# Optimization experiments

Hardware: AMD Instinct MI355X
Metric: run time of the kernel (lower is better)

Reference implementation:

```python
import jax, jax.numpy as jnp
import numpy as np

B, T, D = 2, 2048, 2048
H, KVH, HD = 32, 8, 64
N_REP = H // KVH


def setup_inputs() -> dict:
    key = jax.random.key(0)
    ks = jax.random.split(key, 7)
    x = jax.random.normal(ks[0], (B, T, D), dtype=jnp.float32)
    # rope tables: [max_seq, head_dim//2]
    cos = jax.random.uniform(ks[1], (T, HD // 2), dtype=jnp.float32, minval=-1.0, maxval=1.0)
    sin = jax.random.uniform(ks[2], (T, HD // 2), dtype=jnp.float32, minval=-1.0, maxval=1.0)
    s = 0.02
    wq = jax.random.normal(ks[3], (D, H * HD), dtype=jnp.float32) * s
    wk = jax.random.normal(ks[4], (D, KVH * HD), dtype=jnp.float32) * s
    wv = jax.random.normal(ks[5], (D, KVH * HD), dtype=jnp.float32) * s
    wo = jax.random.normal(ks[6], (H * HD, D), dtype=jnp.float32) * s
    return {"x": x, "cos": cos, "sin": sin, "wq": wq, "wk": wk, "wv": wv, "wo": wo}


def _rotate(t):
    h = t.shape[-1] // 2
    return jnp.concatenate([-t[..., h:], t[..., :h]], axis=-1)


def reference(x, cos, sin, wq, wk, wv, wo):
    b, t, _ = x.shape
    # projections -> [B, heads, T, HD]
    q = (x @ wq).reshape(b, t, H, HD).transpose(0, 2, 1, 3)
    k = (x @ wk).reshape(b, t, KVH, HD).transpose(0, 2, 1, 3)
    v = (x @ wv).reshape(b, t, KVH, HD).transpose(0, 2, 1, 3)
    # rope: cos/sin tiled (concat) to full head_dim, broadcast over batch/head
    cos_f = jnp.tile(cos[:t], (1, 2))[None, None]  # [1,1,T,HD]
    sin_f = jnp.tile(sin[:t], (1, 2))[None, None]
    q = q * cos_f + _rotate(q) * sin_f
    k = k * cos_f + _rotate(k) * sin_f
    # GQA: repeat kv heads
    k = jnp.repeat(k, N_REP, axis=1)
    v = jnp.repeat(v, N_REP, axis=1)
    scale = 1.0 / np.sqrt(HD).astype(np.float32)
    scores = jnp.einsum('bhqd,bhkd->bhqk', q, k) * scale
    causal = jnp.tril(jnp.ones((t, t), dtype=bool))
    scores = jnp.where(causal, scores, jnp.float32(-1e30))
    attn = jax.nn.softmax(scores, axis=-1)
    out = jnp.einsum('bhqk,bhkd->bhqd', attn, v)
    out = out.transpose(0, 2, 1, 3).reshape(b, t, H * HD)
    return out @ wo
```

## Files before the change

kernel.cpp:

```cpp
#include <hip/hip_runtime.h>
#include <hip/hip_bf16.h>
#include <cstdint>

typedef unsigned short u16;
typedef unsigned int u32;
typedef __bf16 bf16x8 __attribute__((ext_vector_type(8)));
typedef float f32x4 __attribute__((ext_vector_type(4)));
typedef float f32x16 __attribute__((ext_vector_type(16)));

#define BATCH 2
#define SEQ 2048
#define DMODEL 2048
#define NH 32
#define NKVH 8
#define HD 64
#define NQROWS (BATCH*SEQ)
#define QCOLS (NH*HD)
#define KVCOLS (NKVH*HD)
#define NCAT (QCOLS+2*KVCOLS)

static __device__ __forceinline__ u16 f2bf(float f) {
  u32 u = __float_as_uint(f);
  return (u16)((u + 0x7fffu + ((u >> 16) & 1u)) >> 16);
}

#define GLOAD16(gp, lp) __builtin_amdgcn_global_load_lds( \
    (const __attribute__((address_space(1))) void*)(gp),  \
    (__attribute__((address_space(3))) void*)(lp), 16, 0, 0)

__global__ __launch_bounds__(256) void k_cvt_bf16(const float* __restrict__ in,
                                                  u16* __restrict__ out, int n4) {
  int i = blockIdx.x * 256 + threadIdx.x;
  if (i >= n4) return;
  float4 v = reinterpret_cast<const float4*>(in)[i];
  ushort4 o;
  o.x = f2bf(v.x); o.y = f2bf(v.y); o.z = f2bf(v.z); o.w = f2bf(v.w);
  reinterpret_cast<ushort4*>(out)[i] = o;
}

__global__ __launch_bounds__(256) void k_transpose_all(const float* __restrict__ wq,
                                                       const float* __restrict__ wk,
                                                       const float* __restrict__ wv,
                                                       const float* __restrict__ wo,
                                                       u16* __restrict__ wcatT,
                                                       u16* __restrict__ woT) {
  __shared__ float tile[32][33];
  const int tidx = blockIdx.x;
  const float* src; u16* dst; int C, c0, r0;
  if (tidx < 4096) {
    src = wq; dst = wcatT; C = QCOLS;
    c0 = (tidx & 63) * 32; r0 = (tidx >> 6) * 32;
  } else if (tidx < 5120) {
    int t2 = tidx - 4096;
    src = wk; dst = wcatT + (size_t)QCOLS * DMODEL; C = KVCOLS;
    c0 = (t2 & 15) * 32; r0 = (t2 >> 4) * 32;
  } else if (tidx < 6144) {
    int t2 = tidx - 5120;
    src = wv; dst = wcatT + (size_t)(QCOLS + KVCOLS) * DMODEL; C = KVCOLS;
    c0 = (t2 & 15) * 32; r0 = (t2 >> 4) * 32;
  } else {
    int t2 = tidx - 6144;
    src = wo; dst = woT; C = DMODEL;
    c0 = (t2 & 63) * 32; r0 = (t2 >> 6) * 32;
  }
  const int R = 2048;
  int tx = threadIdx.x & 31, ty = threadIdx.x >> 5;
#pragma unroll
  for (int i = 0; i < 4; i++)
    tile[ty * 4 + i][tx] = src[(size_t)(r0 + ty * 4 + i) * C + c0 + tx];
  __syncthreads();
#pragma unroll
  for (int i = 0; i < 4; i++)
    dst[(size_t)(c0 + ty * 4 + i) * R + r0 + tx] = f2bf(tile[tx][ty * 4 + i]);
}

template<int EPI>
__global__ __launch_bounds__(256) void k_gemm(const u16* __restrict__ A,
                                              const u16* __restrict__ BT,
                                              void* __restrict__ Cout,
                                              int M, int N, int K,
                                              const float* __restrict__ cosb,
                                              const float* __restrict__ sinb,
                                              u16* __restrict__ dstK,
                                              u16* __restrict__ dstV) {
  __shared__ __align__(16) u16 As[2][128 * 32];
  __shared__ __align__(16) u16 Bs[2][128 * 32];
  const int tid = threadIdx.x;
  const int w = tid >> 6, l = tid & 63;
  const int l15 = l & 15, l4 = l >> 4;

  const int nwg = gridDim.x * gridDim.y;
  int hwid = blockIdx.y * gridDim.x + blockIdx.x;
  int wk = (hwid & 7) * (nwg >> 3) + (hwid >> 3);
  const int bx = wk % gridDim.x, by = wk / gridDim.x;

  const int m0 = by * 128, n0 = bx * 128;
  const int wr = w >> 1, wc = w & 1;

  const u16* ga = A + (size_t)(m0 + w * 32 + (l >> 2)) * K + (l & 3) * 8;
  const u16* gb = BT + (size_t)(n0 + w * 32 + (l >> 2)) * K + (l & 3) * 8;
  const int af_off = (wr * 64 + l15) * 32 + l4 * 8;
  const int bf_off = (wc * 64 + l15) * 32 + l4 * 8;

  auto stage = [&](int buf, int kt) {
    const u16* ga_ = ga + kt;
    const u16* gb_ = gb + kt;
    u16* asb = &As[buf][w * 1024];
    u16* bsb = &Bs[buf][w * 1024];
    GLOAD16(ga_, asb);
    GLOAD16(ga_ + 16 * (size_t)K, asb + 512);
    GLOAD16(gb_, bsb);
    GLOAD16(gb_ + 16 * (size_t)K, bsb + 512);
  };

  f32x4 acc[4][4] = {};
  stage(0, 0);
  __syncthreads();

  int cur = 0;
  for (int kt = 0; kt < K; kt += 32) {
    if (kt + 32 < K) stage(cur ^ 1, kt + 32);
    bf16x8 af[4], bfv[4];
#pragma unroll
    for (int mi = 0; mi < 4; mi++)
      af[mi] = *reinterpret_cast<const bf16x8*>(&As[cur][af_off + mi * 512]);
#pragma unroll
    for (int ni = 0; ni < 4; ni++)
      bfv[ni] = *reinterpret_cast<const bf16x8*>(&Bs[cur][bf_off + ni * 512]);
#pragma unroll
    for (int mi = 0; mi < 4; mi++)
#pragma unroll
      for (int ni = 0; ni < 4; ni++)
        acc[mi][ni] = __builtin_amdgcn_mfma_f32_16x16x32_bf16(af[mi], bfv[ni], acc[mi][ni], 0, 0, 0);
    __syncthreads();
    cur ^= 1;
  }

  const int row0 = m0 + wr * 64 + l4 * 4;
  const int col0 = n0 + wc * 64 + l15;
  if constexpr (EPI == 1) {
    float* C = (float*)Cout;
#pragma unroll
    for (int mi = 0; mi < 4; mi++)
#pragma unroll
      for (int ni = 0; ni < 4; ni++)
#pragma unroll
        for (int j = 0; j < 4; j++)
          C[(size_t)(row0 + mi * 16 + j) * N + col0 + ni * 16] = acc[mi][ni][j];
  } else {
    if (n0 < QCOLS + KVCOLS) {
#pragma unroll
      for (int mi = 0; mi < 4; mi++)
#pragma unroll
        for (int j = 0; j < 4; j++) {
          int t = (row0 + mi * 16 + j) & (SEQ - 1);
#pragma unroll
          for (int ni = 0; ni < 2; ni++) {
            int d = ni * 16 + l15;
            float c = cosb[t * 32 + d], s = sinb[t * 32 + d];
            float a = acc[mi][ni][j], bb = acc[mi][ni + 2][j];
            acc[mi][ni][j]     = a * c - bb * s;
            acc[mi][ni + 2][j] = bb * c + a * s;
          }
        }
      if (n0 < QCOLS) {
        const float QSC = 0.125f * 1.44269504088896f;
        u16* C = (u16*)Cout;
#pragma unroll
        for (int mi = 0; mi < 4; mi++)
#pragma unroll
          for (int ni = 0; ni < 4; ni++)
#pragma unroll
            for (int j = 0; j < 4; j++)
              C[(size_t)(row0 + mi * 16 + j) * QCOLS + col0 + ni * 16] = f2bf(acc[mi][ni][j] * QSC);
      } else {
        int kc0 = col0 - QCOLS;
#pragma unroll
        for (int mi = 0; mi < 4; mi++)
#pragma unroll
          for (int ni = 0; ni < 4; ni++)
#pragma unroll
            for (int j = 0; j < 4; j++)
              dstK[(size_t)(row0 + mi * 16 + j) * KVCOLS + kc0 + ni * 16] = f2bf(acc[mi][ni][j]);
      }
    } else {
      int vc0 = col0 - (QCOLS + KVCOLS);
#pragma unroll
      for (int mi = 0; mi < 4; mi++) {
        int row = row0 + mi * 16;
        int b = row >> 11, t = row & (SEQ - 1);
#pragma unroll
        for (int ni = 0; ni < 4; ni++) {
          ushort4 v;
          v.x = f2bf(acc[mi][ni][0]);
          v.y = f2bf(acc[mi][ni][1]);
          v.z = f2bf(acc[mi][ni][2]);
          v.w = f2bf(acc[mi][ni][3]);
          *reinterpret_cast<ushort4*>(&dstV[((size_t)b * KVCOLS + vc0 + ni * 16) * SEQ + t]) = v;
        }
      }
    }
  }
}

__global__ __launch_bounds__(64, 3) void k_attn(const u16* __restrict__ Q,
                                                const u16* __restrict__ K,
                                                const u16* __restrict__ VT,
                                                u16* __restrict__ AO) {
  __shared__ __align__(16) u16 Ks[2][2048];
  __shared__ __align__(16) u16 Vs[2][2048];
  const int l = threadIdx.x;
  const int lo = l & 31, hi = l >> 5;
  const int id = blockIdx.y * gridDim.x + blockIdx.x;
  const int bh = (id & 7) * 8 + ((id >> 3) & 7);
  const int bxx = id >> 6;
  const int b = bh >> 5, h = bh & 31, g = h >> 2;

  const u16* Kbase = K + ((size_t)b * SEQ) * KVCOLS + g * 64;
  const u16* Vbase = VT + ((size_t)(b * KVCOLS + g * 64)) * SEQ;

  const int ksrow = l >> 3, kscol = l & 7;
  const int kcs = kscol ^ ksrow;
  const int vsrow = l >> 2, vscol = l & 3;
  const int vcs = vscol ^ (vsrow & 3);

  auto stage = [&](int kc, int buf) {
#pragma unroll
    for (int i = 0; i < 4; i++) {
      GLOAD16(Kbase + (size_t)(kc * 32 + i * 8 + ksrow) * KVCOLS + kcs * 8,
              &Ks[buf][i * 512 + l * 8]);
      GLOAD16(Vbase + (size_t)(i * 16 + vsrow) * SEQ + kc * 32 + vcs * 8,
              &Vs[buf][i * 512 + l * 8]);
    }
  };

  for (int half = 0; half < 2; half++) {
    const int qt = half ? (63 - bxx) : bxx;
    const int q0 = qt * 32;
    const int nkc = qt + 1;

    bf16x8 qf[4];
    {
      const u16* qp = Q + (size_t)(b * SEQ + q0 + lo) * QCOLS + h * 64 + hi * 8;
#pragma unroll
      for (int kb = 0; kb < 4; kb++)
        qf[kb] = *reinterpret_cast<const bf16x8*>(qp + kb * 16);
    }
    f32x16 oacc[2] = {};
    float ls = 0.f;

    stage(0, 0);
    int bi = 0;
    for (int kc = 0; kc < nkc; kc++) {
      if (kc + 1 < nkc) {
        stage(kc + 1, bi ^ 1);
        asm volatile("s_waitcnt vmcnt(8)" ::: "memory");
      } else {
        asm volatile("s_waitcnt vmcnt(0)" ::: "memory");
      }
      __builtin_amdgcn_sched_barrier(0);

      f32x16 sacc = {};
      __builtin_amdgcn_s_setprio(1);
#pragma unroll
      for (int kb = 0; kb < 4; kb++) {
        int slot = (2 * kb + hi) ^ (lo & 7);
        bf16x8 kf = *reinterpret_cast<const bf16x8*>(&Ks[bi][lo * 64 + slot * 8]);
        sacc = __builtin_amdgcn_mfma_f32_32x32x16_bf16(kf, qf[kb], sacc, 0, 0, 0);
      }
      __builtin_amdgcn_s_setprio(0);

      const bool diag = (kc == qt);
      float pv[16];
#pragma unroll
      for (int r = 0; r < 16; r++) {
        float e = exp2f(sacc[r]);
        if (diag) {
          int kvg = kc * 32 + (r & 3) + 8 * (r >> 2) + 4 * hi;
          if (kvg > q0 + lo) e = 0.f;
        }
        pv[r] = e; ls += e;
      }
      u32 u[4][2];
#pragma unroll
      for (int qd = 0; qd < 4; qd++)
#pragma unroll
        for (int hh = 0; hh < 2; hh++) {
          u32 uu;
          asm("v_cvt_pk_bf16_f32 %0, %1, %2"
              : "=v"(uu) : "v"(pv[qd * 4 + 2 * hh]), "v"(pv[qd * 4 + 2 * hh + 1]));
          u[qd][hh] = uu;
        }

#pragma unroll
      for (int km = 0; km < 2; km++) {
        u32 a0 = u[2 * km][0], b0 = u[2 * km + 1][0];
        u32 a1 = u[2 * km][1], b1 = u[2 * km + 1][1];
        asm("v_permlane32_swap_b32 %0, %1" : "+v"(a0), "+v"(b0));
        asm("v_permlane32_swap_b32 %0, %1" : "+v"(a1), "+v"(b1));
        union { u32 uu[4]; bf16x8 v; } pa;
        pa.uu[0] = a0; pa.uu[1] = a1; pa.uu[2] = b0; pa.uu[3] = b1;
        __builtin_amdgcn_s_setprio(1);
#pragma unroll
        for (int td = 0; td < 2; td++) {
          int row = td * 32 + lo;
          int slot = (2 * km + hi) ^ (lo & 3);
          bf16x8 vf = *reinterpret_cast<const bf16x8*>(&Vs[bi][row * 32 + slot * 8]);
          oacc[td] = __builtin_amdgcn_mfma_f32_32x32x16_bf16(pa.v, vf, oacc[td], 0, 0, 0);
        }
        __builtin_amdgcn_s_setprio(0);
      }
      bi ^= 1;
    }
    float tot = ls;
    tot += __shfl_xor(tot, 32);
#pragma unroll
    for (int r = 0; r < 16; r++) {
      int qr = (r & 3) + 8 * (r >> 2) + 4 * hi;
      float den = __shfl(tot, qr);
      float rv = __builtin_amdgcn_rcpf(den);
      size_t rowbase = (size_t)(b * SEQ + q0 + qr) * QCOLS + h * 64 + lo;
      AO[rowbase]      = f2bf(oacc[0][r] * rv);
      AO[rowbase + 32] = f2bf(oacc[1][r] * rv);
    }
  }
}

extern "C" void kernel_launch(void* const* d_in, const int* in_sizes, int n_in,
                              void* d_out, int out_size, void* d_ws, size_t ws_size,
                              hipStream_t stream) {
  const float* x    = (const float*)d_in[0];
  const float* cosb = (const float*)d_in[1];
  const float* sinb = (const float*)d_in[2];
  const float* wq   = (const float*)d_in[3];
  const float* wk   = (const float*)d_in[4];
  const float* wv   = (const float*)d_in[5];
  const float* wo   = (const float*)d_in[6];
  float* out = (float*)d_out;

  char* ws = (char*)d_ws;
  size_t off = 0;
  auto alloc = [&](size_t bytes) -> void* {
    void* p = ws + off;
    off += (bytes + 255) & ~(size_t)255;
    return p;
  };
  u16* xb    = (u16*)alloc((size_t)NQROWS * DMODEL * 2);
  u16* wcatT = (u16*)alloc((size_t)NCAT * DMODEL * 2);
  u16* woT   = (u16*)alloc((size_t)DMODEL * QCOLS * 2);
  u16* Qb    = (u16*)alloc((size_t)NQROWS * QCOLS * 2);
  u16* Kb    = (u16*)alloc((size_t)NQROWS * KVCOLS * 2);
  u16* VTb   = (u16*)alloc((size_t)BATCH * KVCOLS * SEQ * 2);
  u16* AO    = (u16*)alloc((size_t)NQROWS * QCOLS * 2);

  k_cvt_bf16<<<dim3(NQROWS * DMODEL / 4 / 256), dim3(256), 0, stream>>>(x, xb, NQROWS * DMODEL / 4);
  k_transpose_all<<<dim3(10240), dim3(256), 0, stream>>>(wq, wk, wv, wo, wcatT, woT);

  k_gemm<3><<<dim3(NCAT / 128, NQROWS / 128), 256, 0, stream>>>(
      xb, wcatT, Qb, NQROWS, NCAT, DMODEL, cosb, sinb, Kb, VTb);

  k_attn<<<dim3(32, BATCH * NH), 64, 0, stream>>>(Qb, Kb, VTb, AO);

  k_gemm<1><<<dim3(DMODEL / 128, NQROWS / 128), 256, 0, stream>>>(
      AO, woT, out, NQROWS, DMODEL, QCOLS, nullptr, nullptr, nullptr, nullptr);
}
```

Baseline: 229.0 us.

## Restructure causal attention into two-wave blocks with balanced dual KV streams

```diff
diff --git a/kernel.cpp b/kernel.cpp
--- a/kernel.cpp
+++ b/kernel.cpp
@@ -203,13 +203,14 @@
   }
 }
 
-__global__ __launch_bounds__(64, 3) void k_attn(const u16* __restrict__ Q,
-                                                const u16* __restrict__ K,
-                                                const u16* __restrict__ VT,
-                                                u16* __restrict__ AO) {
-  __shared__ __align__(16) u16 Ks[2][2048];
-  __shared__ __align__(16) u16 Vs[2][2048];
-  const int l = threadIdx.x;
+__global__ __launch_bounds__(128, 2) void k_attn(const u16* __restrict__ Q,
+                                                 const u16* __restrict__ K,
+                                                 const u16* __restrict__ VT,
+                                                 u16* __restrict__ AO) {
+  __shared__ __align__(16) u16 Ks[2][2][2048];
+  __shared__ __align__(16) u16 Vs[2][2][2048];
+  const int tid = threadIdx.x;
+  const int w = tid >> 6, l = tid & 63;
   const int lo = l & 31, hi = l >> 5;
   const int id = blockIdx.y * gridDim.x + blockIdx.x;
   const int bh = (id & 7) * 8 + ((id >> 3) & 7);
@@ -219,109 +220,131 @@
   const u16* Kbase = K + ((size_t)b * SEQ) * KVCOLS + g * 64;
   const u16* Vbase = VT + ((size_t)(b * KVCOLS + g * 64)) * SEQ;
 
-  const int ksrow = l >> 3, kscol = l & 7;
-  const int kcs = kscol ^ ksrow;
-  const int vsrow = l >> 2, vscol = l & 3;
-  const int vcs = vscol ^ (vsrow & 3);
-
-  auto stage = [&](int kc, int buf) {
-#pragma unroll
-    for (int i = 0; i < 4; i++) {
-      GLOAD16(Kbase + (size_t)(kc * 32 + i * 8 + ksrow) * KVCOLS + kcs * 8,
-              &Ks[buf][i * 512 + l * 8]);
-      GLOAD16(Vbase + (size_t)(i * 16 + vsrow) * SEQ + kc * 32 + vcs * 8,
-              &Vs[buf][i * 512 + l * 8]);
+  const int qtA = bxx, qtB = 31 - bxx;
+  const int q0A = qtA * 64 + w * 32;
+  const int q0B = qtB * 64 + w * 32;
+  const int nA = 2 * bxx + 2;
+  const int c2base = 33 - nA;
+
+  const int k_r = l >> 3, k_cs = (l & 7) ^ (l >> 3);
+  const int v_r = l >> 2, v_cs = (l & 3) ^ ((l >> 2) & 3);
+
+  auto stage = [&](int s, int bi, int c) {
+#pragma unroll
+    for (int i = 0; i < 2; i++) {
+      GLOAD16(Kbase + (size_t)(c * 32 + w * 16 + i * 8 + k_r) * KVCOLS + k_cs * 8,
+              &Ks[s][bi][(w * 16 + i * 8) * 64 + l * 8]);
+      GLOAD16(Vbase + (size_t)(w * 32 + i * 16 + v_r) * SEQ + c * 32 + v_cs * 8,
+              &Vs[s][bi][(w * 32 + i * 16) * 32 + l * 8]);
     }
   };
-
-  for (int half = 0; half < 2; half++) {
-    const int qt = half ? (63 - bxx) : bxx;
-    const int q0 = qt * 32;
-    const int nkc = qt + 1;
-
-    bf16x8 qf[4];
-    {
-      const u16* qp = Q + (size_t)(b * SEQ + q0 + lo) * QCOLS + h * 64 + hi * 8;
-#pragma unroll
-      for (int kb = 0; kb < 4; kb++)
-        qf[kb] = *reinterpret_cast<const bf16x8*>(qp + kb * 16);
-    }
-    f32x16 oacc[2] = {};
-    float ls = 0.f;
-
-    stage(0, 0);
-    int bi = 0;
-    for (int kc = 0; kc < nkc; kc++) {
-      if (kc + 1 < nkc) {
-        stage(kc + 1, bi ^ 1);
-        asm volatile("s_waitcnt vmcnt(8)" ::: "memory");
-      } else {
-        asm volatile("s_waitcnt vmcnt(0)" ::: "memory");
-      }
-      __builtin_amdgcn_sched_barrier(0);
-
-      f32x16 sacc = {};
+  auto c1_of = [&](int j) { return j < nA ? j : j - nA; };
+
+  bf16x8 qfA[4], qfB[4];
+  {
+    const u16* qpA = Q + (size_t)(b * SEQ + q0A + lo) * QCOLS + h * 64 + hi * 8;
+    const u16* qpB = Q + (size_t)(b * SEQ + q0B + lo) * QCOLS + h * 64 + hi * 8;
+#pragma unroll
+    for (int kb = 0; kb < 4; kb++) {
+      qfA[kb] = *reinterpret_cast<const bf16x8*>(qpA + kb * 16);
+      qfB[kb] = *reinterpret_cast<const bf16x8*>(qpB + kb * 16);
+    }
+  }
+  f32x16 oaccA[2] = {}, oaccB[2] = {};
+  float lsA = 0.f, lsB = 0.f;
+
+  auto chain = [&](int s, int bi, int c, const bf16x8* qf, f32x16* oacc,
+                   float& ls, int qt, int q0) {
+    f32x16 sacc = {};
+    __builtin_amdgcn_s_setprio(1);
+#pragma unroll
+    for (int kb = 0; kb < 4; kb++) {
+      int slot = (2 * kb + hi) ^ (lo & 7);
+      bf16x8 kf = *reinterpret_cast<const bf16x8*>(&Ks[s][bi][lo * 64 + slot * 8]);
+      sacc = __builtin_amdgcn_mfma_f32_32x32x16_bf16(kf, qf[kb], sacc, 0, 0, 0);
+    }
+    __builtin_amdgcn_s_setprio(0);
+    const bool msk = (c >= 2 * qt);
+    float pv[16];
+#pragma unroll
+    for (int r = 0; r < 16; r++) {
+      float e = exp2f(sacc[r]);
+      if (msk) {
+        int kvg = c * 32 + (r & 3) + 8 * (r >> 2) + 4 * hi;
+        if (kvg > q0 + lo) e = 0.f;
+      }
+      pv[r] = e; ls += e;
+    }
+    u32 u[4][2];
+#pragma unroll
+    for (int qd = 0; qd < 4; qd++)
+#pragma unroll
+      for (int hh = 0; hh < 2; hh++) {
+        u32 uu;
+        asm("v_cvt_pk_bf16_f32 %0, %1, %2"
+            : "=v"(uu) : "v"(pv[qd * 4 + 2 * hh]), "v"(pv[qd * 4 + 2 * hh + 1]));
+        u[qd][hh] = uu;
+      }
+#pragma unroll
+    for (int km = 0; km < 2; km++) {
+      u32 a0 = u[2 * km][0], b0 = u[2 * km + 1][0];
+      u32 a1 = u[2 * km][1], b1 = u[2 * km + 1][1];
+      asm("v_permlane32_swap_b32 %0, %1" : "+v"(a0), "+v"(b0));
+      asm("v_permlane32_swap_b32 %0, %1" : "+v"(a1), "+v"(b1));
+      union { u32 uu[4]; bf16x8 v; } pa;
+      pa.uu[0] = a0; pa.uu[1] = a1; pa.uu[2] = b0; pa.uu[3] = b1;
       __builtin_amdgcn_s_setprio(1);
 #pragma unroll
-      for (int kb = 0; kb < 4; kb++) {
-        int slot = (2 * kb + hi) ^ (lo & 7);
-        bf16x8 kf = *reinterpret_cast<const bf16x8*>(&Ks[bi][lo * 64 + slot * 8]);
-        sacc = __builtin_amdgcn_mfma_f32_32x32x16_bf16(kf, qf[kb], sacc, 0, 0, 0);
+      for (int td = 0; td < 2; td++) {
+        int row = td * 32 + lo;
+        int slot = (2 * km + hi) ^ (row & 3);
+        bf16x8 vf = *reinterpret_cast<const bf16x8*>(&Vs[s][bi][row * 32 + slot * 8]);
+        oacc[td] = __builtin_amdgcn_mfma_f32_32x32x16_bf16(pa.v, vf, oacc[td], 0, 0, 0);
       }
       __builtin_amdgcn_s_setprio(0);
-
-      const bool diag = (kc == qt);
-      float pv[16];
-#pragma unroll
-      for (int r = 0; r < 16; r++) {
-        float e = exp2f(sacc[r]);
-        if (diag) {
-          int kvg = kc * 32 + (r & 3) + 8 * (r >> 2) + 4 * hi;
-          if (kvg > q0 + lo) e = 0.f;
-        }
-        pv[r] = e; ls += e;
-      }
-      u32 u[4][2];
-#pragma unroll
-      for (int qd = 0; qd < 4; qd++)
-#pragma unroll
-        for (int hh = 0; hh < 2; hh++) {
-          u32 uu;
-          asm("v_cvt_pk_bf16_f32 %0, %1, %2"
-              : "=v"(uu) : "v"(pv[qd * 4 + 2 * hh]), "v"(pv[qd * 4 + 2 * hh + 1]));
-          u[qd][hh] = uu;
-        }
-
-#pragma unroll
-      for (int km = 0; km < 2; km++) {
-        u32 a0 = u[2 * km][0], b0 = u[2 * km + 1][0];
-        u32 a1 = u[2 * km][1], b1 = u[2 * km + 1][1];
-        asm("v_permlane32_swap_b32 %0, %1" : "+v"(a0), "+v"(b0));
-        asm("v_permlane32_swap_b32 %0, %1" : "+v"(a1), "+v"(b1));
-        union { u32 uu[4]; bf16x8 v; } pa;
-        pa.uu[0] = a0; pa.uu[1] = a1; pa.uu[2] = b0; pa.uu[3] = b1;
-        __builtin_amdgcn_s_setprio(1);
-#pragma unroll
-        for (int td = 0; td < 2; td++) {
-          int row = td * 32 + lo;
-          int slot = (2 * km + hi) ^ (lo & 3);
-          bf16x8 vf = *reinterpret_cast<const bf16x8*>(&Vs[bi][row * 32 + slot * 8]);
-          oacc[td] = __builtin_amdgcn_mfma_f32_32x32x16_bf16(pa.v, vf, oacc[td], 0, 0, 0);
-        }
-        __builtin_amdgcn_s_setprio(0);
-      }
-      bi ^= 1;
-    }
-    float tot = ls;
+    }
+  };
+
+  stage(0, 0, c1_of(0));
+  stage(1, 0, c2base);
+  __syncthreads();
+
+  for (int j = 0; j < 33; j++) {
+    const int bi = j & 1;
+    if (j + 1 < 33) {
+      stage(0, bi ^ 1, c1_of(j + 1));
+      stage(1, bi ^ 1, c2base + j + 1);
+    }
+    if (j < nA) chain(0, bi, j, qfA, oaccA, lsA, qtA, q0A);
+    else        chain(0, bi, j - nA, qfB, oaccB, lsB, qtB, q0B);
+    chain(1, bi, c2base + j, qfB, oaccB, lsB, qtB, q0B);
+    __syncthreads();
+  }
+
+  {
+    float tot = lsA;
     tot += __shfl_xor(tot, 32);
 #pragma unroll
     for (int r = 0; r < 16; r++) {
       int qr = (r & 3) + 8 * (r >> 2) + 4 * hi;
       float den = __shfl(tot, qr);
       float rv = __builtin_amdgcn_rcpf(den);
-      size_t rowbase = (size_t)(b * SEQ + q0 + qr) * QCOLS + h * 64 + lo;
-      AO[rowbase]      = f2bf(oacc[0][r] * rv);
-      AO[rowbase + 32] = f2bf(oacc[1][r] * rv);
+      size_t rowbase = (size_t)(b * SEQ + q0A + qr) * QCOLS + h * 64 + lo;
+      AO[rowbase]      = f2bf(oaccA[0][r] * rv);
+      AO[rowbase + 32] = f2bf(oaccA[1][r] * rv);
+    }
+  }
+  {
+    float tot = lsB;
+    tot += __shfl_xor(tot, 32);
+#pragma unroll
+    for (int r = 0; r < 16; r++) {
+      int qr = (r & 3) + 8 * (r >> 2) + 4 * hi;
+      float den = __shfl(tot, qr);
+      float rv = __builtin_amdgcn_rcpf(den);
+      size_t rowbase = (size_t)(b * SEQ + q0B + qr) * QCOLS + h * 64 + lo;
+      AO[rowbase]      = f2bf(oaccB[0][r] * rv);
+      AO[rowbase + 32] = f2bf(oaccB[1][r] * rv);
     }
   }
 }
@@ -359,7 +382,7 @@
   k_gemm<3><<<dim3(NCAT / 128, NQROWS / 128), 256, 0, stream>>>(
       xb, wcatT, Qb, NQROWS, NCAT, DMODEL, cosb, sinb, Kb, VTb);
 
-  k_attn<<<dim3(32, BATCH * NH), 64, 0, stream>>>(Qb, Kb, VTb, AO);
+  k_attn<<<dim3(16, BATCH * NH), 128, 0, stream>>>(Qb, Kb, VTb, AO);
 
   k_gemm<1><<<dim3(DMODEL / 128, NQROWS / 128), 256, 0, stream>>>(
       AO, woT, out, NQROWS, DMODEL, QCOLS, nullptr, nullptr, nullptr, nullptr);
```

Measured after the change: 215.8 us. 5.7% less time.
